# Optimization experiments

Measured on AMD Instinct MI355X. Metric: run time of the kernel, lower is better.

Reference implementation:

```python
import jax, jax.numpy as jnp
import numpy as np

TEMP = 0.5
EPS = 1e-8  # torch CosineSimilarity eps


def setup_inputs() -> dict:
    key = jax.random.key(0)
    k1, k2 = jax.random.split(key)
    B, D = 4096, 256
    return {
        "features1": jax.random.normal(k1, (B, D), dtype=jnp.float32),
        "features2": jax.random.normal(k2, (B, D), dtype=jnp.float32),
    }


def reference(features1, features2):
    B = features1.shape[0]
    f = jnp.concatenate([features1, features2], axis=0)  # [2B, D]
    # cosine similarity matrix via norms + GEMM (same math as broadcasted cos)
    n = jnp.sqrt(jnp.sum(f * f, axis=-1))  # [2B]
    dots = f @ f.T  # [2B, 2B]
    logits = dots / jnp.maximum(n[:, None] * n[None, :], EPS) / TEMP
    # labels = cat([arange(B), arange(B)]) -- faithful to the source module
    labels = jnp.concatenate([jnp.arange(B), jnp.arange(B)], axis=0)  # [2B]
    lse = jax.nn.logsumexp(logits, axis=1)  # [2B]
    picked = logits[jnp.arange(2 * B), labels]  # [2B]
    return jnp.mean(lse - picked)
```

## Files before the change

### kernel.cpp

```cpp
#include <hip/hip_runtime.h>
#include <hip/hip_bf16.h>
#include <math.h>


#define B_ROWS 4096
#define D_DIM  256
#define N_ROWS 8192
#define NPANEL 64

typedef __attribute__((ext_vector_type(8))) short short8;
typedef __attribute__((ext_vector_type(4))) float f32x4;

__global__ __launch_bounds__(256) void nt_norm_picked(
    const float* __restrict__ f1, const float* __restrict__ f2,
    unsigned short* __restrict__ G, float* __restrict__ picked_cross,
    float* __restrict__ prow) {
  __shared__ float4 vbuf[2][64];
  __shared__ float ssbuf[2];
  const int tid = threadIdx.x, lane = tid & 63, w = tid >> 6;
  const int zidx = blockIdx.x * 256 + tid;
  if (zidx < 32768) reinterpret_cast<float4*>(prow)[zidx] = float4{0.f, 0.f, 0.f, 0.f};
  const int pl = w >> 1, src = w & 1;
  const int p = blockIdx.x * 2 + pl;
  const float* rowp = (src == 0 ? f1 : f2) + (size_t)p * D_DIM;
  float4 v = reinterpret_cast<const float4*>(rowp)[lane];
  float ss = v.x * v.x + v.y * v.y + v.z * v.z + v.w * v.w;
#pragma unroll
  for (int m = 1; m < 64; m <<= 1) ss += __shfl_xor(ss, m, 64);
  const float scale = 1.41421356237309515f * rsqrtf(fmaxf(ss, 1e-30f));
  union { ushort4 u; __hip_bfloat16 h[4]; } pk;
  pk.h[0] = __float2bfloat16(v.x * scale);
  pk.h[1] = __float2bfloat16(v.y * scale);
  pk.h[2] = __float2bfloat16(v.z * scale);
  pk.h[3] = __float2bfloat16(v.w * scale);
  const int grow = p + src * B_ROWS;
  reinterpret_cast<ushort4*>(G + (size_t)grow * D_DIM)[lane] = pk.u;
  if (src == 0) { vbuf[pl][lane] = v; if (lane == 0) ssbuf[pl] = ss; }
  __syncthreads();
  if (src == 1) {
    float4 u = vbuf[pl][lane];
    float d = v.x * u.x + v.y * u.y + v.z * u.z + v.w * u.w;
#pragma unroll
    for (int m = 1; m < 64; m <<= 1) d += __shfl_xor(d, m, 64);
    if (lane == 0)
      picked_cross[p] = 2.0f * d * rsqrtf(ss) * rsqrtf(ssbuf[pl]);
  }
}

__device__ __forceinline__ void stage_lds(const char* gsrc_base, char* lds_base,
                                          int tid) {
  const int lane = tid & 63, wid = tid >> 6;
#pragma unroll
  for (int r = 0; r < 8; ++r) {
    const int o  = r * 4096 + wid * 1024 + lane * 16;
    const int so = o ^ (((o >> 9) & 7) << 4);
    __builtin_amdgcn_global_load_lds(
        (const __attribute__((address_space(1))) void*)(gsrc_base + so),
        (__attribute__((address_space(3))) void*)(lds_base + r * 4096 + wid * 1024),
        16, 0, 0);
  }
}

__global__ __launch_bounds__(256, 2) void nt_gemm_tri(
    const unsigned short* __restrict__ G,
    float* __restrict__ prow,
    float* __restrict__ pcol)
{
  const int bid = blockIdx.x;
  const int p   = bid & 31;
  const int k   = bid >> 5;
  const int rbA = 63 - p;
  const int n1  = 2 * (rbA + 1);
  const int t0  = (130 * k) >> 4;
  const int t1  = (130 * (k + 1)) >> 4;

  const int tid = threadIdx.x, lane = tid & 63, wid = tid >> 6;
  const int wr = wid >> 1, wc = wid & 1;
  const int l15 = lane & 15, q16 = (lane >> 4) << 4;

  __shared__ short8 lds8[4096];
  char* ldsb = reinterpret_cast<char*>(lds8);
  const char* gb = reinterpret_cast<const char*>(G);

  int rb = (t0 < n1) ? rbA : p;
  stage_lds(gb + (t0 < n1 ? t0 : t0 - n1) * 32768, ldsb, tid);

  short8 af[4][8];
#pragma unroll
  for (int m = 0; m < 4; ++m) {
    const int ro = (rb * 128 + wr * 64 + m * 16 + l15) * 512;
#pragma unroll
    for (int ks = 0; ks < 8; ++ks) {
      af[m][ks] = *reinterpret_cast<const short8*>(gb + ro + ks * 64 + q16);
      asm volatile("" : "+v"(af[m][ks]));
    }
  }
  float rs[16];
#pragma unroll
  for (int i = 0; i < 16; ++i) rs[i] = 0.f;
  __syncthreads();

  for (int t = t0; t < t1; ++t) {
    char* bbuf = ldsb + ((t - t0) & 1) * 32768;
    if (t + 1 < t1) {
      const int sbn = (t + 1 < n1) ? t + 1 : t + 1 - n1;
      stage_lds(gb + sbn * 32768, ldsb + ((t + 1 - t0) & 1) * 32768, tid);
    }
    const int sb = (t < n1) ? t : t - n1;

    f32x4 acc[4][2] = {};
#pragma unroll
    for (int ks = 0; ks < 8; ++ks) {
      short8 bf[2];
#pragma unroll
      for (int n = 0; n < 2; ++n) {
        const int brow = wc * 32 + n * 16 + l15;
        const int off  = (brow * 512 + ks * 64 + q16) ^ ((brow & 7) << 4);
        bf[n] = *reinterpret_cast<const short8*>(bbuf + off);
      }
#pragma unroll
      for (int m = 0; m < 4; ++m)
#pragma unroll
        for (int n = 0; n < 2; ++n)
          acc[m][n] = __builtin_amdgcn_mfma_f32_16x16x32_bf16(
              af[m][ks], bf[n], acc[m][n], 0, 0, 0);
    }

    float cs0 = 0.f, cs1 = 0.f;
#pragma unroll
    for (int m = 0; m < 4; ++m)
#pragma unroll
      for (int j = 0; j < 4; ++j) {
        const float e0 = __expf(acc[m][0][j]);
        const float e1 = __expf(acc[m][1][j]);
        rs[m * 4 + j] += e0 + e1;
        cs0 += e0; cs1 += e1;
      }
    if ((sb >> 1) != rb) {
      cs0 += __shfl_xor(cs0, 16, 64); cs0 += __shfl_xor(cs0, 32, 64);
      cs1 += __shfl_xor(cs1, 16, 64); cs1 += __shfl_xor(cs1, 32, 64);
      if (lane < 16) {
        float* dst = pcol + (size_t)(2 * rb + wr) * N_ROWS + sb * 64 + wc * 32 + lane;
        dst[0]  = cs0;
        dst[16] = cs1;
      }
    }

    const bool last = (t + 1 == t1);
    const bool swi  = (t + 1 == n1) && !last;
    if (last || swi) {
#pragma unroll
      for (int i = 0; i < 16; ++i) {
        float v = rs[i];
        v += __shfl_xor(v, 1, 64);
        v += __shfl_xor(v, 2, 64);
        v += __shfl_xor(v, 4, 64);
        v += __shfl_xor(v, 8, 64);
        rs[i] = v;
      }
      if (l15 == 0) {
        const int g = lane >> 4;
#pragma unroll
        for (int i = 0; i < 16; ++i)
          atomicAdd(&prow[(size_t)k * N_ROWS + rb * 128 + wr * 64 +
                          (i >> 2) * 16 + g * 4 + (i & 3)], rs[i]);
      }
#pragma unroll
      for (int i = 0; i < 16; ++i) rs[i] = 0.f;
    }
    if (swi) {
      rb = p;
#pragma unroll
      for (int m = 0; m < 4; ++m) {
        const int ro = (rb * 128 + wr * 64 + m * 16 + l15) * 512;
#pragma unroll
        for (int ks = 0; ks < 8; ++ks) {
          af[m][ks] = *reinterpret_cast<const short8*>(gb + ro + ks * 64 + q16);
          asm volatile("" : "+v"(af[m][ks]));
        }
      }
    }
    __syncthreads();
  }
}

__global__ __launch_bounds__(256) void nt_finalize1(
    const float* __restrict__ prow, const float* __restrict__ pcol,
    const float* __restrict__ picked_cross, float* __restrict__ loss_part) {
  const int blk = blockIdx.x, tid = threadIdx.x;
  const int pan = blk >> 1;
  const int l   = tid & 63;
  const int r   = pan * 128 + (blk & 1) * 64 + l;
  const int g   = tid >> 6;
  float s = 0.f;
  if (g == 0) {
#pragma unroll
    for (int j = 0; j < 16; ++j) s += prow[(size_t)j * N_ROWS + r];
  } else {
    for (int rb = pan + g; rb < NPANEL; rb += 3) {
      s += pcol[(size_t)(2 * rb) * N_ROWS + r];
      s += pcol[(size_t)(2 * rb + 1) * N_ROWS + r];
    }
  }
  __shared__ float red[4][64];
  red[g][l] = s;
  __syncthreads();
  if (g == 0) {
    float tot = red[0][l] + red[1][l] + red[2][l] + red[3][l];
    const float pick = (r < B_ROWS) ? 2.0f : picked_cross[r - B_ROWS];
    float local = __logf(tot) - pick;
#pragma unroll
    for (int m = 1; m < 64; m <<= 1) local += __shfl_xor(local, m, 64);
    if (l == 0) loss_part[blk] = local;
  }
}

__global__ __launch_bounds__(128) void nt_finalize2(
    const float* __restrict__ loss_part, float* __restrict__ out) {
  const int tid = threadIdx.x;
  float v = loss_part[tid];
#pragma unroll
  for (int m = 1; m < 64; m <<= 1) v += __shfl_xor(v, m, 64);
  __shared__ float red[2];
  if ((tid & 63) == 0) red[tid >> 6] = v;
  __syncthreads();
  if (tid == 0) out[0] = (red[0] + red[1]) / (float)N_ROWS;
}

extern "C" void kernel_launch(void* const* d_in, const int* in_sizes, int n_in,
                              void* d_out, int out_size, void* d_ws, size_t ws_size,
                              hipStream_t stream) {
  const float* f1 = (const float*)d_in[0];
  const float* f2 = (const float*)d_in[1];
  float* out = (float*)d_out;

  char* ws = (char*)d_ws;
  unsigned short* G   = (unsigned short*)ws;
  float* prow         = (float*)(ws + (size_t)4 * 1024 * 1024);
  float* pcol         = (float*)(ws + (size_t)5 * 1024 * 1024);
  float* picked_cross = (float*)(ws + (size_t)9 * 1024 * 1024);
  float* loss_part    = (float*)(ws + (size_t)9 * 1024 * 1024 + 64 * 1024);

  hipLaunchKernelGGL(nt_norm_picked, dim3(B_ROWS / 2), dim3(256), 0, stream,
                     f1, f2, G, picked_cross, prow);
  hipLaunchKernelGGL(nt_gemm_tri, dim3(512), dim3(256), 0, stream,
                     G, prow, pcol);
  hipLaunchKernelGGL(nt_finalize1, dim3(128), dim3(256), 0, stream,
                     prow, pcol, picked_cross, loss_part);
  hipLaunchKernelGGL(nt_finalize2, dim3(1), dim3(128), 0, stream,
                     loss_part, out);
}
```

Measured before the change: 58.80 us.

## Switch similarity GEMM to FP8 operands and double the K-split grid

Normalized rows are quantized to FP8 (e4m3) instead of bf16, and the GEMM uses the fp8 MFMA with halved LDS staging, byte offsets and swizzle. The triangular workload is split across 32 chunks instead of 16, giving 1024 workgroups at 4 per CU with an XCD-aware block remap. The partial-row buffer and finalize loop grow to match. This halves operand bandwidth and LDS footprint and raises occupancy, at the cost of lower precision in the exponentiated logits.

```diff
diff --git a/kernel.cpp b/kernel.cpp
--- a/kernel.cpp
+++ b/kernel.cpp
@@ -7,19 +7,19 @@
 #define D_DIM  256
 #define N_ROWS 8192
 #define NPANEL 64
-
-typedef __attribute__((ext_vector_type(8))) short short8;
+#define NSPLIT 32
+
 typedef __attribute__((ext_vector_type(4))) float f32x4;
 
 __global__ __launch_bounds__(256) void nt_norm_picked(
     const float* __restrict__ f1, const float* __restrict__ f2,
-    unsigned short* __restrict__ G, float* __restrict__ picked_cross,
+    unsigned char* __restrict__ G, float* __restrict__ picked_cross,
     float* __restrict__ prow) {
   __shared__ float4 vbuf[2][64];
   __shared__ float ssbuf[2];
   const int tid = threadIdx.x, lane = tid & 63, w = tid >> 6;
   const int zidx = blockIdx.x * 256 + tid;
-  if (zidx < 32768) reinterpret_cast<float4*>(prow)[zidx] = float4{0.f, 0.f, 0.f, 0.f};
+  if (zidx < 65536) reinterpret_cast<float4*>(prow)[zidx] = float4{0.f, 0.f, 0.f, 0.f};
   const int pl = w >> 1, src = w & 1;
   const int p = blockIdx.x * 2 + pl;
   const float* rowp = (src == 0 ? f1 : f2) + (size_t)p * D_DIM;
@@ -28,13 +28,10 @@
 #pragma unroll
   for (int m = 1; m < 64; m <<= 1) ss += __shfl_xor(ss, m, 64);
   const float scale = 1.41421356237309515f * rsqrtf(fmaxf(ss, 1e-30f));
-  union { ushort4 u; __hip_bfloat16 h[4]; } pk;
-  pk.h[0] = __float2bfloat16(v.x * scale);
-  pk.h[1] = __float2bfloat16(v.y * scale);
-  pk.h[2] = __float2bfloat16(v.z * scale);
-  pk.h[3] = __float2bfloat16(v.w * scale);
+  int wpk = __builtin_amdgcn_cvt_pk_fp8_f32(v.x * scale, v.y * scale, 0, false);
+  wpk     = __builtin_amdgcn_cvt_pk_fp8_f32(v.z * scale, v.w * scale, wpk, true);
   const int grow = p + src * B_ROWS;
-  reinterpret_cast<ushort4*>(G + (size_t)grow * D_DIM)[lane] = pk.u;
+  reinterpret_cast<int*>(G + (size_t)grow * D_DIM)[lane] = wpk;
   if (src == 0) { vbuf[pl][lane] = v; if (lane == 0) ssbuf[pl] = ss; }
   __syncthreads();
   if (src == 1) {
@@ -51,9 +48,9 @@
                                           int tid) {
   const int lane = tid & 63, wid = tid >> 6;
 #pragma unroll
-  for (int r = 0; r < 8; ++r) {
+  for (int r = 0; r < 4; ++r) {
     const int o  = r * 4096 + wid * 1024 + lane * 16;
-    const int so = o ^ (((o >> 9) & 7) << 4);
+    const int so = o ^ (((o >> 8) & 7) << 4);
     __builtin_amdgcn_global_load_lds(
         (const __attribute__((address_space(1))) void*)(gsrc_base + so),
         (__attribute__((address_space(3))) void*)(lds_base + r * 4096 + wid * 1024),
@@ -61,68 +58,72 @@
   }
 }
 
-__global__ __launch_bounds__(256, 2) void nt_gemm_tri(
-    const unsigned short* __restrict__ G,
+__device__ __forceinline__ void load_af(const char* gb, int rb, int wr,
+                                        int l15, int q8, long af[4][8]) {
+#pragma unroll
+  for (int m = 0; m < 4; ++m) {
+    const int ro = (rb * 128 + wr * 64 + m * 16 + l15) * 256;
+#pragma unroll
+    for (int ks = 0; ks < 8; ++ks)
+      af[m][ks] = *reinterpret_cast<const long*>(gb + ro + ks * 32 + q8);
+  }
+}
+
+__global__ __launch_bounds__(256, 4) void nt_gemm_tri(
+    const unsigned char* __restrict__ G,
     float* __restrict__ prow,
     float* __restrict__ pcol)
 {
-  const int bid = blockIdx.x;
-  const int p   = bid & 31;
-  const int k   = bid >> 5;
+  const int wg  = (blockIdx.x & 7) * 128 + (blockIdx.x >> 3);
+  const int p   = wg >> 5;
+  const int k   = wg & 31;
   const int rbA = 63 - p;
   const int n1  = 2 * (rbA + 1);
-  const int t0  = (130 * k) >> 4;
-  const int t1  = (130 * (k + 1)) >> 4;
+  const int t0  = (130 * k) >> 5;
+  const int t1  = (130 * (k + 1)) >> 5;
 
   const int tid = threadIdx.x, lane = tid & 63, wid = tid >> 6;
   const int wr = wid >> 1, wc = wid & 1;
-  const int l15 = lane & 15, q16 = (lane >> 4) << 4;
-
-  __shared__ short8 lds8[4096];
+  const int l15 = lane & 15, q8 = (lane >> 4) << 3;
+
+  __shared__ long lds8[4096];
   char* ldsb = reinterpret_cast<char*>(lds8);
   const char* gb = reinterpret_cast<const char*>(G);
 
   int rb = (t0 < n1) ? rbA : p;
-  stage_lds(gb + (t0 < n1 ? t0 : t0 - n1) * 32768, ldsb, tid);
-
-  short8 af[4][8];
-#pragma unroll
-  for (int m = 0; m < 4; ++m) {
-    const int ro = (rb * 128 + wr * 64 + m * 16 + l15) * 512;
-#pragma unroll
-    for (int ks = 0; ks < 8; ++ks) {
-      af[m][ks] = *reinterpret_cast<const short8*>(gb + ro + ks * 64 + q16);
-      asm volatile("" : "+v"(af[m][ks]));
-    }
-  }
+  stage_lds(gb + (size_t)(t0 < n1 ? t0 : t0 - n1) * 16384, ldsb, tid);
+
+  long af[4][8];
+  load_af(gb, rb, wr, l15, q8, af);
+
   float rs[16];
 #pragma unroll
   for (int i = 0; i < 16; ++i) rs[i] = 0.f;
   __syncthreads();
 
   for (int t = t0; t < t1; ++t) {
-    char* bbuf = ldsb + ((t - t0) & 1) * 32768;
+    char* bbuf = ldsb + ((t - t0) & 1) * 16384;
     if (t + 1 < t1) {
       const int sbn = (t + 1 < n1) ? t + 1 : t + 1 - n1;
-      stage_lds(gb + sbn * 32768, ldsb + ((t + 1 - t0) & 1) * 32768, tid);
+      stage_lds(gb + (size_t)sbn * 16384, ldsb + ((t + 1 - t0) & 1) * 16384, tid);
     }
     const int sb = (t < n1) ? t : t - n1;
 
     f32x4 acc[4][2] = {};
 #pragma unroll
     for (int ks = 0; ks < 8; ++ks) {
-      short8 bf[2];
+      long bf[2];
 #pragma unroll
       for (int n = 0; n < 2; ++n) {
         const int brow = wc * 32 + n * 16 + l15;
-        const int off  = (brow * 512 + ks * 64 + q16) ^ ((brow & 7) << 4);
-        bf[n] = *reinterpret_cast<const short8*>(bbuf + off);
+        const int off  = (brow * 256 + ks * 32 + q8) ^ ((brow & 7) << 4);
+        bf[n] = *reinterpret_cast<const long*>(bbuf + off);
       }
 #pragma unroll
       for (int m = 0; m < 4; ++m)
 #pragma unroll
         for (int n = 0; n < 2; ++n)
-          acc[m][n] = __builtin_amdgcn_mfma_f32_16x16x32_bf16(
+          acc[m][n] = __builtin_amdgcn_mfma_f32_16x16x32_fp8_fp8(
               af[m][ks], bf[n], acc[m][n], 0, 0, 0);
     }
 
@@ -170,15 +171,7 @@
     }
     if (swi) {
       rb = p;
-#pragma unroll
-      for (int m = 0; m < 4; ++m) {
-        const int ro = (rb * 128 + wr * 64 + m * 16 + l15) * 512;
-#pragma unroll
-        for (int ks = 0; ks < 8; ++ks) {
-          af[m][ks] = *reinterpret_cast<const short8*>(gb + ro + ks * 64 + q16);
-          asm volatile("" : "+v"(af[m][ks]));
-        }
-      }
+      load_af(gb, rb, wr, l15, q8, af);
     }
     __syncthreads();
   }
@@ -195,7 +188,7 @@
   float s = 0.f;
   if (g == 0) {
 #pragma unroll
-    for (int j = 0; j < 16; ++j) s += prow[(size_t)j * N_ROWS + r];
+    for (int j = 0; j < NSPLIT; ++j) s += prow[(size_t)j * N_ROWS + r];
   } else {
     for (int rb = pan + g; rb < NPANEL; rb += 3) {
       s += pcol[(size_t)(2 * rb) * N_ROWS + r];
@@ -235,15 +228,15 @@
   float* out = (float*)d_out;
 
   char* ws = (char*)d_ws;
-  unsigned short* G   = (unsigned short*)ws;
-  float* prow         = (float*)(ws + (size_t)4 * 1024 * 1024);
-  float* pcol         = (float*)(ws + (size_t)5 * 1024 * 1024);
-  float* picked_cross = (float*)(ws + (size_t)9 * 1024 * 1024);
-  float* loss_part    = (float*)(ws + (size_t)9 * 1024 * 1024 + 64 * 1024);
+  unsigned char* G    = (unsigned char*)ws;
+  float* prow         = (float*)(ws + (size_t)2 * 1024 * 1024);
+  float* pcol         = (float*)(ws + (size_t)3 * 1024 * 1024);
+  float* picked_cross = (float*)(ws + (size_t)7 * 1024 * 1024);
+  float* loss_part    = (float*)(ws + (size_t)7 * 1024 * 1024 + 64 * 1024);
 
   hipLaunchKernelGGL(nt_norm_picked, dim3(B_ROWS / 2), dim3(256), 0, stream,
                      f1, f2, G, picked_cross, prow);
-  hipLaunchKernelGGL(nt_gemm_tri, dim3(512), dim3(256), 0, stream,
+  hipLaunchKernelGGL(nt_gemm_tri, dim3(1024), dim3(256), 0, stream,
                      G, prow, pcol);
   hipLaunchKernelGGL(nt_finalize1, dim3(128), dim3(256), 0, stream,
                      prow, pcol, picked_cross, loss_part);
```

Result: slower. 82.49 us (+40.3%).
